# Kernel tuning notes

Hardware: AMD Instinct MI355X
Metric: run time of the kernel (lower is better)

## Reference

```python
import jax, jax.numpy as jnp
import numpy as np

B, L, S, H, E, M = 16, 2048, 2048, 8, 64, 64  # batch, q len, kv len, heads, per-head dim, modes
SCALE = 1.0 / (512 * 512)  # 1/(in_channels*out_channels)


def setup_inputs() -> dict:
    key = jax.random.key(0)
    kq, kk, kv, kw1, kw2 = jax.random.split(key, 5)
    return {
        "q": jax.random.normal(kq, (B, L, H, E), dtype=jnp.float32),
        "k": jax.random.normal(kk, (B, S, H, E), dtype=jnp.float32),
        "v": jax.random.normal(kv, (B, S, H, E), dtype=jnp.float32),
        "weights_real": SCALE * jax.random.uniform(kw1, (H, E, E, M), dtype=jnp.float32),
        "weights_imag": SCALE * jax.random.uniform(kw2, (H, E, E, M), dtype=jnp.float32),
        "mask": jnp.zeros((1,), dtype=bool),  # unused by forward (kept for signature parity)
    }


def reference(q, k, v, weights_real, weights_imag, mask):
    # [B, L, H, E] -> [B, H, E, L]
    _q = jnp.transpose(q, (0, 2, 3, 1))
    _k = jnp.transpose(k, (0, 2, 3, 1))
    _v = jnp.transpose(v, (0, 2, 3, 1))

    # rFFT along time; mode_select_method='else' => index = range(M), a contiguous slice
    Qf = jnp.fft.rfft(_q, axis=-1)[..., :M]  # [B, H, E, M] complex
    Kf = jnp.fft.rfft(_k, axis=-1)[..., :M]
    Vf = jnp.fft.rfft(_v, axis=-1)[..., :M]

    # cross attention in frequency domain
    QK = jnp.einsum('bhex,bhey->bhxy', Qf, Kf)  # [B, H, M, M] complex
    QK = jnp.tanh(QK.real) + 1j * jnp.tanh(QK.imag)  # 'tanh' activation on re/im
    QKV = jnp.einsum('bhxy,bhey->bhex', QK, Vf)  # [B, H, E, M]

    W = (weights_real + 1j * weights_imag).astype(jnp.complex64)  # [H, E, O, M]
    QKVW = jnp.einsum('bhex,heox->bhox', QKV, W)  # [B, H, O, M]

    # scatter selected modes back into full half-spectrum, then inverse FFT
    Y = jnp.zeros((B, H, E, L // 2 + 1), dtype=jnp.complex64).at[..., :M].set(QKVW)
    y = jnp.fft.irfft(Y, n=L, axis=-1)  # [B, H, O, L] real
    return jnp.transpose(y, (0, 3, 1, 2))  # [B, L, H, O]
```

## Files before the change

### kernel.cpp

```cpp
#include <hip/hip_runtime.h>
#include <hip/hip_fp16.h>
#include <math.h>


#define NB 16
#define NL 2048
#define NH 8
#define NE 64
#define NM 64
#define NHE 512

typedef unsigned short ushort_t;
typedef __attribute__((ext_vector_type(8))) short short8;
typedef __attribute__((ext_vector_type(8))) _Float16 half8;
typedef __attribute__((ext_vector_type(4))) float f32x4;

__device__ inline void gld_lds16(const void* g, void* l) {
    __builtin_amdgcn_global_load_lds((const __attribute__((address_space(1))) unsigned int*)g,
                                     (__attribute__((address_space(3))) unsigned int*)l, 16, 0, 0);
}

__global__ __launch_bounds__(256) void k_tables(ushort_t* __restrict__ Twh,
                                                ushort_t* __restrict__ Twl,
                                                ushort_t* __restrict__ Ih) {
    const int blk = blockIdx.x;
    if (blk < 1024) {
        int i = blk * 256 + threadIdx.x;
        int kj = i & 7;
        int l  = (i >> 3) & 63;
        int g  = (i >> 9) & 7;
        int ks = i >> 12;
        int mp = g * 16 + (l & 15);
        int kk = (l >> 4) * 8 + kj;
        int t = ks * 32 + kk;
        int m = mp >> 1;
        float ang = (float)((6.283185307179586476925287 / (double)NL) * (double)((m * t) & (NL - 1)));
        float val = (mp & 1) ? -sinf(ang) : cosf(ang);
        unsigned cb = __float_as_uint(val);
        ushort_t h = (ushort_t)(cb >> 16);
        float lo = val - __uint_as_float(cb & 0xffff0000u);
        unsigned lb = __float_as_uint(lo);
        unsigned r = lb + 0x7fffu + ((lb >> 16) & 1u);
        Twh[i] = h;
        Twl[i] = (ushort_t)(r >> 16);
    } else {
        int i = (blk - 1024) * 256 + threadIdx.x;
        int j = i & 7;
        int l = (i >> 3) & 63;
        int f = (i >> 9) & 15;
        int ks = (i >> 13) & 3;
        int tt = i >> 15;
        int t = tt * 256 + f * 16 + (l & 15);
        int kk = ks * 32 + (l >> 4) * 8 + j;
        int x = kk >> 1;
        float ang = (float)((6.283185307179586476925287 / (double)NL) * (double)((t * x) & (NL - 1)));
        float val = (kk & 1) ? -sinf(ang) : cosf(ang);
        Ih[i] = __half_as_ushort(__float2half(val));
    }
}

__global__ __launch_bounds__(256, 3) void k_gemm(
    const float* __restrict__ q, const float* __restrict__ k, const float* __restrict__ v,
    const ushort_t* __restrict__ Twh, const ushort_t* __restrict__ Twl,
    float* __restrict__ Part) {
    const int bx = blockIdx.x & 7;
    const int kq = blockIdx.x >> 3;
    const int b  = blockIdx.y;
    const int z  = blockIdx.z;
    const float* __restrict__ in = (z == 0) ? q : ((z == 1) ? k : v);

    const int tid  = threadIdx.x;
    const int wid  = tid >> 6;
    const int lane = tid & 63;
    const int lr   = lane & 15;
    const int lg   = lane >> 4;
    const int wy   = wid >> 1;
    const int wx   = wid & 1;
    const int he0  = bx * 64;
    const int fx   = lg & 1;

    __shared__ float    As[2][32 * 64];
    __shared__ ushort_t Bh[2][4096];
    __shared__ ushort_t Bl[2][4096];

    f32x4 acc[2][4];
#pragma unroll
    for (int f = 0; f < 2; ++f)
#pragma unroll
        for (int j = 0; j < 4; ++j) acc[f][j] = (f32x4){0.f, 0.f, 0.f, 0.f};

    const size_t in_blk = ((size_t)b * NL + (size_t)kq * 1024) * NHE + he0;

#define STAGE(n, ksn)                                                                 \
    {                                                                                 \
        const ushort_t* gh = Twh + (size_t)(kq * 32 + (ksn)) * 4096;                  \
        const ushort_t* gl = Twl + (size_t)(kq * 32 + (ksn)) * 4096;                  \
        gld_lds16(gh + (size_t)tid * 8, &Bh[n][tid * 8]);                             \
        gld_lds16(gh + (size_t)(tid + 256) * 8, &Bh[n][(tid + 256) * 8]);             \
        gld_lds16(gl + (size_t)tid * 8, &Bl[n][tid * 8]);                             \
        gld_lds16(gl + (size_t)(tid + 256) * 8, &Bl[n][(tid + 256) * 8]);             \
        const float* ga = in + in_blk + (size_t)(ksn) * 32 * NHE;                     \
        _Pragma("unroll")                                                             \
        for (int p = 0; p < 2; ++p) {                                                 \
            int u = tid + p * 256;                                                    \
            int tloc = u >> 4, hc = u & 15;                                           \
            int hcs = hc ^ (((tloc >> 3) & 1) << 2);                                  \
            gld_lds16(ga + (size_t)tloc * NHE + hcs * 4, &As[n][u * 4]);              \
        }                                                                             \
    }

    STAGE(0, 0);

    int cur = 0;
    for (int ks = 0; ks < 32; ++ks) {
        __syncthreads();
        if (ks + 1 < 32) STAGE(cur ^ 1, ks + 1);

        const float* ac = &As[cur][0];
        const ushort_t* bhc = &Bh[cur][0];
        const ushort_t* blc = &Bl[cur][0];

        short8 bh8[4], bl8[4];
#pragma unroll
        for (int j = 0; j < 4; ++j) {
            bh8[j] = *(const short8*)&bhc[((wx * 4 + j) * 64 + lane) * 8];
            bl8[j] = *(const short8*)&blc[((wx * 4 + j) * 64 + lane) * 8];
        }

#pragma unroll
        for (int f = 0; f < 2; ++f) {
            const int col = wy * 32 + ((f ^ fx) << 4) + lr;
            float xa[8];
#pragma unroll
            for (int j = 0; j < 8; ++j) xa[j] = ac[(8 * lg + j) * 64 + col];
            union { unsigned u[4]; short8 s; } uh, ul;
#pragma unroll
            for (int p = 0; p < 4; ++p) {
                unsigned b0 = __float_as_uint(xa[2 * p]);
                unsigned b1 = __float_as_uint(xa[2 * p + 1]);
                uh.u[p] = (b0 >> 16) | (b1 & 0xffff0000u);
                float l0 = xa[2 * p]     - __uint_as_float(b0 & 0xffff0000u);
                float l1 = xa[2 * p + 1] - __uint_as_float(b1 & 0xffff0000u);
                unsigned lw;
                asm("v_cvt_pk_bf16_f32 %0, %1, %2" : "=v"(lw) : "v"(l0), "v"(l1));
                ul.u[p] = lw;
            }
#pragma unroll
            for (int j = 0; j < 4; ++j) {
                acc[f][j] = __builtin_amdgcn_mfma_f32_16x16x32_bf16(uh.s, bh8[j], acc[f][j], 0, 0, 0);
                acc[f][j] = __builtin_amdgcn_mfma_f32_16x16x32_bf16(ul.s, bh8[j], acc[f][j], 0, 0, 0);
                acc[f][j] = __builtin_amdgcn_mfma_f32_16x16x32_bf16(uh.s, bl8[j], acc[f][j], 0, 0, 0);
            }
        }
        cur ^= 1;
    }
#undef STAGE

    float* pout = Part + (size_t)(z * 2 + kq) * 1048576;
#pragma unroll
    for (int f = 0; f < 2; ++f) {
#pragma unroll
        for (int j = 0; j < 4; ++j) {
            const int col = wx * 64 + j * 16 + lr;
#pragma unroll
            for (int r = 0; r < 4; ++r) {
                const int he = he0 + wy * 32 + f * 16 + 4 * lg + r;
                pout[((size_t)b * NHE + he) * 128 + col] = acc[f][j][r];
            }
        }
    }
}

__global__ __launch_bounds__(512) void k_qkqkv(
    const float* __restrict__ Part, float2* __restrict__ QKV) {
    const int bh = blockIdx.x;
    const int xh = blockIdx.y;
    const int tid = threadIdx.x;

    __shared__ float2 bufA[64 * 34];
    __shared__ float2 bufB[64 * 66];

    const float4* P0 = (const float4*)Part;
    const float4* P1 = P0 + 262144;
    const float4* P2 = P0 + 2 * 262144;
    const float4* P3 = P0 + 3 * 262144;
    const float4* P4 = P0 + 4 * 262144;
    const float4* P5 = P0 + 5 * 262144;
    const size_t fb = (size_t)bh * 2048;

#pragma unroll
    for (int j = 0; j < 2; ++j) {
        int n = tid + j * 512;
        int e = n >> 4, c = n & 15;
        float4 a = P0[fb + e * 32 + xh * 16 + c];
        float4 b = P1[fb + e * 32 + xh * 16 + c];
        *((float4*)&bufA[e * 34 + c * 2]) =
            make_float4(a.x + b.x, a.y + b.y, a.z + b.z, a.w + b.w);
    }
#pragma unroll
    for (int j = 0; j < 4; ++j) {
        int n = tid + j * 512;
        int e = n >> 5, c = n & 31;
        float4 a = P2[fb + e * 32 + c];
        float4 b = P3[fb + e * 32 + c];
        *((float4*)&bufB[e * 66 + c * 2]) =
            make_float4(a.x + b.x, a.y + b.y, a.z + b.z, a.w + b.w);
    }
    __syncthreads();

    const int yq = tid & 31, xq = tid >> 5;
    const int x0 = xq * 2;
    float accr[2][2], acci[2][2];
#pragma unroll
    for (int i = 0; i < 2; ++i)
#pragma unroll
        for (int j = 0; j < 2; ++j) { accr[i][j] = 0.f; acci[i][j] = 0.f; }

    for (int e = 0; e < 64; ++e) {
        float4 qa = *((float4*)&bufA[e * 34 + x0]);
        float4 kk = *((float4*)&bufB[e * 66 + yq * 2]);
        float qr[2] = {qa.x, qa.z};
        float qi[2] = {qa.y, qa.w};
        float kr[2] = {kk.x, kk.z};
        float ki[2] = {kk.y, kk.w};
#pragma unroll
        for (int i = 0; i < 2; ++i) {
#pragma unroll
            for (int j = 0; j < 2; ++j) {
                accr[i][j] += qr[i] * kr[j] - qi[i] * ki[j];
                acci[i][j] += qr[i] * ki[j] + qi[i] * kr[j];
            }
        }
    }
    __syncthreads();

    float2* Ps = bufA;
#pragma unroll
    for (int i = 0; i < 2; ++i) {
        float4 sv = make_float4(tanhf(accr[i][0]), tanhf(acci[i][0]),
                                tanhf(accr[i][1]), tanhf(acci[i][1]));
        *((float4*)&Ps[(x0 + i) * 66 + yq * 2]) = sv;
    }
#pragma unroll
    for (int j = 0; j < 4; ++j) {
        int n = tid + j * 512;
        int e = n >> 5, c = n & 31;
        float4 a = P4[fb + e * 32 + c];
        float4 b = P5[fb + e * 32 + c];
        *((float4*)&bufB[e * 66 + c * 2]) =
            make_float4(a.x + b.x, a.y + b.y, a.z + b.z, a.w + b.w);
    }
    __syncthreads();

    const int xq2 = tid & 7, eq2 = tid >> 3;
    const int x2 = xq2 * 4;
    float br[4], bi[4];
#pragma unroll
    for (int j = 0; j < 4; ++j) { br[j] = 0.f; bi[j] = 0.f; }

    for (int yy = 0; yy < 64; ++yy) {
        float2 v0 = bufB[eq2 * 66 + yy];
        float2 p0 = Ps[(x2 + 0) * 66 + yy];
        float2 p1 = Ps[(x2 + 1) * 66 + yy];
        float2 p2 = Ps[(x2 + 2) * 66 + yy];
        float2 p3 = Ps[(x2 + 3) * 66 + yy];
        float pr[4] = {p0.x, p1.x, p2.x, p3.x};
        float pi[4] = {p0.y, p1.y, p2.y, p3.y};
#pragma unroll
        for (int j = 0; j < 4; ++j) {
            br[j] += v0.x * pr[j] - v0.y * pi[j];
            bi[j] += v0.x * pi[j] + v0.y * pr[j];
        }
    }
    {
        float2* obase = QKV + (size_t)bh * 4096 + eq2 * 64 + xh * 32 + x2;
        float4 s0 = make_float4(br[0], bi[0], br[1], bi[1]);
        float4 s1 = make_float4(br[2], bi[2], br[3], bi[3]);
        ((float4*)obase)[0] = s0;
        ((float4*)obase)[1] = s1;
    }
}

__global__ __launch_bounds__(256) void k_wt(
    const float* __restrict__ wr, const float* __restrict__ wi,
    float2* __restrict__ Wt) {
    const int e = blockIdx.x, h = blockIdx.y;
    const int tid = threadIdx.x;
    __shared__ float lr[64 * 68];
    __shared__ float li[64 * 68];
    const float* rbase = wr + (size_t)(h * NE + e) * NE * NM;
    const float* ibase = wi + (size_t)(h * NE + e) * NE * NM;
#pragma unroll
    for (int j = 0; j < 4; ++j) {
        int n = tid + j * 256;
        int o = n >> 4, x4 = n & 15;
        float4 r4 = ((const float4*)(rbase + o * NM))[x4];
        float4 i4 = ((const float4*)(ibase + o * NM))[x4];
        *((float4*)&lr[o * 68 + x4 * 4]) = r4;
        *((float4*)&li[o * 68 + x4 * 4]) = i4;
    }
    __syncthreads();
#pragma unroll
    for (int j = 0; j < 16; ++j) {
        int n = tid + j * 256;
        int x = n >> 6, o = n & 63;
        Wt[((size_t)(h * NM + x) * NE + e) * NE + o] =
            make_float2(lr[o * 68 + x], li[o * 68 + x]);
    }
}

__global__ __launch_bounds__(256) void k_qkvw(
    const float2* __restrict__ QKV, const float2* __restrict__ Wt,
    float2* __restrict__ QKVWs) {
    const int x = blockIdx.x, h = blockIdx.y;
    const int tid = threadIdx.x;
    const int o = tid & 63, bq = tid >> 6;
    float accr[4], acci[4];
#pragma unroll
    for (int j = 0; j < 4; ++j) { accr[j] = 0.f; acci[j] = 0.f; }

    const float2* wbase = Wt + (size_t)(h * NM + x) * NE * NE + o;
    for (int e = 0; e < 64; ++e) {
        float2 w = wbase[(size_t)e * NE];
#pragma unroll
        for (int j = 0; j < 4; ++j) {
            int b = bq * 4 + j;
            float2 a = QKV[((size_t)(b * NH + h) * NE + e) * NM + x];
            accr[j] += a.x * w.x - a.y * w.y;
            acci[j] += a.x * w.y + a.y * w.x;
        }
    }
    const float sc = (x == 0) ? 0.5f : 1.0f;
#pragma unroll
    for (int j = 0; j < 4; ++j) {
        int b = bq * 4 + j;
        QKVWs[((size_t)(b * NH + h) * NM + x) * NE + o] =
            make_float2(accr[j] * sc, acci[j] * sc);
    }
}

__global__ __launch_bounds__(256, 3) void k_idft(
    const float2* __restrict__ QKVWs, const ushort_t* __restrict__ Ih,
    float* __restrict__ yout) {
    const int tt = blockIdx.x;
    const int bh = blockIdx.y;
    const int b = bh >> 3, h = bh & 7;
    const int tid = threadIdx.x;
    const int wid = tid >> 6;
    const int lane = tid & 63;
    const int lr = lane & 15;
    const int lg = lane >> 4;

    __shared__ ushort_t Ta[8192];
    __shared__ unsigned Xs[4096];

    const float2* xb = QKVWs + (size_t)bh * 4096;
#pragma unroll
    for (int r = 0; r < 16; ++r) {
        int i = tid + r * 256;
        int x = i >> 6, o = i & 63;
        float2 val = xb[i];
        int ks = x >> 4;
        int lane2 = (((x & 15) >> 2) << 4) | (o & 15);
        int jn = o >> 4;
        unsigned pk = (unsigned)__half_as_ushort(__float2half(val.x)) |
                      ((unsigned)__half_as_ushort(__float2half(val.y)) << 16);
        Xs[((ks * 4 + jn) * 64 + lane2) * 4 + (x & 3)] = pk;
    }
    {
        const ushort_t* gh = Ih + (size_t)(tt * 4) * 8192;
#pragma unroll
        for (int p = 0; p < 4; ++p)
            gld_lds16(gh + (size_t)(tid + p * 256) * 8, &Ta[(tid + p * 256) * 8]);
    }
    __syncthreads();

    f32x4 acc[4][4];
#pragma unroll
    for (int m = 0; m < 4; ++m)
#pragma unroll
        for (int n = 0; n < 4; ++n) acc[m][n] = (f32x4){0.f, 0.f, 0.f, 0.f};

    const ushort_t* XsS = (const ushort_t*)Xs;
    for (int ks = 0; ks < 4; ++ks) {
        half8 ah[4], bx_[4];
#pragma unroll
        for (int m = 0; m < 4; ++m)
            ah[m] = *(const half8*)&Ta[((wid * 4 + m) * 64 + lane) * 8];
#pragma unroll
        for (int n = 0; n < 4; ++n)
            bx_[n] = *(const half8*)&XsS[((ks * 4 + n) * 64 + lane) * 8];
#pragma unroll
        for (int m = 0; m < 4; ++m)
#pragma unroll
            for (int n = 0; n < 4; ++n)
                acc[m][n] = __builtin_amdgcn_mfma_f32_16x16x32_f16(ah[m], bx_[n], acc[m][n], 0, 0, 0);
        if (ks < 3) {
            __syncthreads();
            const ushort_t* gh = Ih + (size_t)(tt * 4 + ks + 1) * 8192;
#pragma unroll
            for (int p = 0; p < 4; ++p)
                gld_lds16(gh + (size_t)(tid + p * 256) * 8, &Ta[(tid + p * 256) * 8]);
            __syncthreads();
        }
    }

    const int t0 = tt * 256 + wid * 64;
    const float inv = 1.f / 1024.f;
#pragma unroll
    for (int m = 0; m < 4; ++m) {
#pragma unroll
        for (int n = 0; n < 4; ++n) {
            const int o = n * 16 + lr;
#pragma unroll
            for (int r = 0; r < 4; ++r) {
                const int t = t0 + m * 16 + lg * 4 + r;
                yout[(((size_t)b * NL + t) * NH + h) * NE + o] = acc[m][n][r] * inv;
            }
        }
    }
}

extern "C" void kernel_launch(void* const* d_in, const int* in_sizes, int n_in,
                              void* d_out, int out_size, void* d_ws, size_t ws_size,
                              hipStream_t stream) {
    const float* q  = (const float*)d_in[0];
    const float* k  = (const float*)d_in[1];
    const float* v  = (const float*)d_in[2];
    const float* wr = (const float*)d_in[3];
    const float* wi = (const float*)d_in[4];
    float* out = (float*)d_out;

    char* w = (char*)d_ws;
    ushort_t* Twh  = (ushort_t*)w;
    ushort_t* Twl  = (ushort_t*)(w + 524288);
    ushort_t* Ih   = (ushort_t*)(w + 1048576);
    float2*   QKV  = (float2*)(w + 2097152);
    float*    Part = (float*)(w + 14680064);
    float2*   Wt   = (float2*)(w + 23068672);
    float2*   QKVWs= (float2*)(w + 39845888);

    hipLaunchKernelGGL(k_tables, dim3(2048), dim3(256), 0, stream, Twh, Twl, Ih);
    hipLaunchKernelGGL(k_gemm, dim3(16, 16, 3), dim3(256), 0, stream,
                       q, k, v, Twh, Twl, Part);
    hipLaunchKernelGGL(k_qkqkv, dim3(128, 2), dim3(512), 0, stream, Part, QKV);
    hipLaunchKernelGGL(k_wt, dim3(64, 8), dim3(256), 0, stream, wr, wi, Wt);
    hipLaunchKernelGGL(k_qkvw, dim3(64, 8), dim3(256), 0, stream, QKV, Wt, QKVWs);
    hipLaunchKernelGGL(k_idft, dim3(8, 128), dim3(256), 0, stream, QKVWs, Ih, out);
}
```

Baseline: 144.7 us.

## Fuse weight transpose into DFT GEMM launch and store weights as packed bf16

The separate weight-transpose kernel is removed and its work becomes an extra z-slice of the forward DFT GEMM grid, so the transpose overlaps with the GEMM blocks and one launch goes away. The transposed complex weights are stored as packed bf16 real/imag pairs in one 32-bit word instead of float2, which halves the bytes k_qkvw reads and writes. The cost is lower weight precision (bf16 rounding) and extra branch logic in the GEMM kernel. Shared memory is reused for the transpose staging.

Result: slower. 178.9 us (+23.6%).

```diff
diff --git a/kernel.cpp b/kernel.cpp
--- a/kernel.cpp
+++ b/kernel.cpp
@@ -18,6 +18,11 @@
 __device__ inline void gld_lds16(const void* g, void* l) {
     __builtin_amdgcn_global_load_lds((const __attribute__((address_space(1))) unsigned int*)g,
                                      (__attribute__((address_space(3))) unsigned int*)l, 16, 0, 0);
+}
+
+__device__ inline unsigned bf16_rne_bits(float v) {
+    unsigned b = __float_as_uint(v);
+    return (b + 0x7fffu + ((b >> 16) & 1u)) >> 16;
 }
 
 __global__ __launch_bounds__(256) void k_tables(ushort_t* __restrict__ Twh,
@@ -39,10 +44,8 @@
         unsigned cb = __float_as_uint(val);
         ushort_t h = (ushort_t)(cb >> 16);
         float lo = val - __uint_as_float(cb & 0xffff0000u);
-        unsigned lb = __float_as_uint(lo);
-        unsigned r = lb + 0x7fffu + ((lb >> 16) & 1u);
         Twh[i] = h;
-        Twl[i] = (ushort_t)(r >> 16);
+        Twl[i] = (ushort_t)bf16_rne_bits(lo);
     } else {
         int i = (blk - 1024) * 256 + threadIdx.x;
         int j = i & 7;
@@ -61,15 +64,57 @@
 
 __global__ __launch_bounds__(256, 3) void k_gemm(
     const float* __restrict__ q, const float* __restrict__ k, const float* __restrict__ v,
+    const float* __restrict__ wr, const float* __restrict__ wi,
     const ushort_t* __restrict__ Twh, const ushort_t* __restrict__ Twl,
-    float* __restrict__ Part) {
+    float* __restrict__ Part, unsigned* __restrict__ Wtb16) {
+    const int b  = blockIdx.y;
+    const int z  = blockIdx.z;
+
+    const int tid  = threadIdx.x;
+
+    __shared__ float    As[2][32 * 64];
+    __shared__ ushort_t Bh[2][4096];
+    __shared__ ushort_t Bl[2][4096];
+
+    if (z == 3) {
+        const int idx = blockIdx.x * 16 + b;
+        const int h = idx & 7, e2 = idx >> 3;
+        float* lr = (float*)&Bh[0][0];
+        float* li = (float*)&Bl[0][0];
+        for (int u = 0; u < 2; ++u) {
+            const int e = e2 * 2 + u;
+            const float* rbase = wr + (size_t)(h * NE + e) * NE * NM;
+            const float* ibase = wi + (size_t)(h * NE + e) * NE * NM;
+            for (int oh = 0; oh < 2; ++oh) {
+#pragma unroll
+                for (int j = 0; j < 2; ++j) {
+                    int n = tid + j * 256;
+                    int o = n >> 4, x4 = n & 15;
+                    float4 r4 = ((const float4*)(rbase + (size_t)(oh * 32 + o) * NM))[x4];
+                    float4 i4 = ((const float4*)(ibase + (size_t)(oh * 32 + o) * NM))[x4];
+                    *((float4*)&lr[o * 68 + x4 * 4]) = r4;
+                    *((float4*)&li[o * 68 + x4 * 4]) = i4;
+                }
+                __syncthreads();
+#pragma unroll
+                for (int j = 0; j < 8; ++j) {
+                    int n = tid + j * 256;
+                    int x = n >> 5, o = n & 31;
+                    unsigned hre = bf16_rne_bits(lr[o * 68 + x]);
+                    unsigned him = bf16_rne_bits(li[o * 68 + x]);
+                    Wtb16[((size_t)(h * NM + x) * NE + e) * NE + oh * 32 + o] =
+                        hre | (him << 16);
+                }
+                __syncthreads();
+            }
+        }
+        return;
+    }
+
     const int bx = blockIdx.x & 7;
     const int kq = blockIdx.x >> 3;
-    const int b  = blockIdx.y;
-    const int z  = blockIdx.z;
     const float* __restrict__ in = (z == 0) ? q : ((z == 1) ? k : v);
 
-    const int tid  = threadIdx.x;
     const int wid  = tid >> 6;
     const int lane = tid & 63;
     const int lr   = lane & 15;
@@ -78,10 +123,6 @@
     const int wx   = wid & 1;
     const int he0  = bx * 64;
     const int fx   = lg & 1;
-
-    __shared__ float    As[2][32 * 64];
-    __shared__ ushort_t Bh[2][4096];
-    __shared__ ushort_t Bl[2][4096];
 
     f32x4 acc[2][4];
 #pragma unroll
@@ -281,36 +322,8 @@
     }
 }
 
-__global__ __launch_bounds__(256) void k_wt(
-    const float* __restrict__ wr, const float* __restrict__ wi,
-    float2* __restrict__ Wt) {
-    const int e = blockIdx.x, h = blockIdx.y;
-    const int tid = threadIdx.x;
-    __shared__ float lr[64 * 68];
-    __shared__ float li[64 * 68];
-    const float* rbase = wr + (size_t)(h * NE + e) * NE * NM;
-    const float* ibase = wi + (size_t)(h * NE + e) * NE * NM;
-#pragma unroll
-    for (int j = 0; j < 4; ++j) {
-        int n = tid + j * 256;
-        int o = n >> 4, x4 = n & 15;
-        float4 r4 = ((const float4*)(rbase + o * NM))[x4];
-        float4 i4 = ((const float4*)(ibase + o * NM))[x4];
-        *((float4*)&lr[o * 68 + x4 * 4]) = r4;
-        *((float4*)&li[o * 68 + x4 * 4]) = i4;
-    }
-    __syncthreads();
-#pragma unroll
-    for (int j = 0; j < 16; ++j) {
-        int n = tid + j * 256;
-        int x = n >> 6, o = n & 63;
-        Wt[((size_t)(h * NM + x) * NE + e) * NE + o] =
-            make_float2(lr[o * 68 + x], li[o * 68 + x]);
-    }
-}
-
 __global__ __launch_bounds__(256) void k_qkvw(
-    const float2* __restrict__ QKV, const float2* __restrict__ Wt,
+    const float2* __restrict__ QKV, const unsigned* __restrict__ Wtb16,
     float2* __restrict__ QKVWs) {
     const int x = blockIdx.x, h = blockIdx.y;
     const int tid = threadIdx.x;
@@ -319,15 +332,18 @@
 #pragma unroll
     for (int j = 0; j < 4; ++j) { accr[j] = 0.f; acci[j] = 0.f; }
 
-    const float2* wbase = Wt + (size_t)(h * NM + x) * NE * NE + o;
+    const unsigned* wbase = Wtb16 + (size_t)(h * NM + x) * NE * NE + o;
+#pragma unroll 8
     for (int e = 0; e < 64; ++e) {
-        float2 w = wbase[(size_t)e * NE];
+        unsigned w = wbase[(size_t)e * NE];
+        float wre = __uint_as_float(w << 16);
+        float wim = __uint_as_float(w & 0xffff0000u);
 #pragma unroll
         for (int j = 0; j < 4; ++j) {
             int b = bq * 4 + j;
             float2 a = QKV[((size_t)(b * NH + h) * NE + e) * NM + x];
-            accr[j] += a.x * w.x - a.y * w.y;
-            acci[j] += a.x * w.y + a.y * w.x;
+            accr[j] += a.x * wre - a.y * wim;
+            acci[j] += a.x * wim + a.y * wre;
         }
     }
     const float sc = (x == 0) ? 0.5f : 1.0f;
@@ -432,19 +448,18 @@
     float* out = (float*)d_out;
 
     char* w = (char*)d_ws;
-    ushort_t* Twh  = (ushort_t*)w;
-    ushort_t* Twl  = (ushort_t*)(w + 524288);
-    ushort_t* Ih   = (ushort_t*)(w + 1048576);
-    float2*   QKV  = (float2*)(w + 2097152);
-    float*    Part = (float*)(w + 14680064);
-    float2*   Wt   = (float2*)(w + 23068672);
-    float2*   QKVWs= (float2*)(w + 39845888);
+    ushort_t* Twh   = (ushort_t*)w;
+    ushort_t* Twl   = (ushort_t*)(w + 524288);
+    ushort_t* Ih    = (ushort_t*)(w + 1048576);
+    float2*   QKV   = (float2*)(w + 2097152);
+    unsigned* Wtb16 = (unsigned*)(w + 6291456);
+    float*    Part  = (float*)(w + 14680064);
+    float2*   QKVWs = (float2*)(w + 39845888);
 
     hipLaunchKernelGGL(k_tables, dim3(2048), dim3(256), 0, stream, Twh, Twl, Ih);
-    hipLaunchKernelGGL(k_gemm, dim3(16, 16, 3), dim3(256), 0, stream,
-                       q, k, v, Twh, Twl, Part);
+    hipLaunchKernelGGL(k_gemm, dim3(16, 16, 4), dim3(256), 0, stream,
+                       q, k, v, wr, wi, Twh, Twl, Part, Wtb16);
     hipLaunchKernelGGL(k_qkqkv, dim3(128, 2), dim3(512), 0, stream, Part, QKV);
-    hipLaunchKernelGGL(k_wt, dim3(64, 8), dim3(256), 0, stream, wr, wi, Wt);
-    hipLaunchKernelGGL(k_qkvw, dim3(64, 8), dim3(256), 0, stream, QKV, Wt, QKVWs);
+    hipLaunchKernelGGL(k_qkvw, dim3(64, 8), dim3(256), 0, stream, QKV, Wtb16, QKVWs);
     hipLaunchKernelGGL(k_idft, dim3(8, 128), dim3(256), 0, stream, QKVWs, Ih, out);
 }
```
